# Kernel tuning notes

Hardware: AMD Instinct MI355X
Metric: run time of the kernel (lower is better)

## Reference

```python
import jax, jax.numpy as jnp
import numpy as np

B, S, M, E, H, F, V, L = 2, 2048, 1024, 512, 8, 2048, 8192, 6


def setup_inputs() -> dict:
    key = jax.random.key(0)
    ks = iter(jax.random.split(key, 32))
    n = lambda shape, s=0.02: jax.random.normal(next(ks), shape, jnp.float32) * s
    return {
        "encoded": jax.random.normal(next(ks), (B, M, E), jnp.float32),
        "seq": jax.random.randint(next(ks), (B, S), 0, V, jnp.int32),
        "input_embed": n((V, E)),           # shared input/output embedding
        "pos_embed": n((S, E)),
        "output_bias": jnp.zeros((V,), jnp.float32),
        "self_in_w": n((L, 3 * E, E)), "self_in_b": jnp.zeros((L, 3 * E), jnp.float32),
        "self_out_w": n((L, E, E)), "self_out_b": jnp.zeros((L, E), jnp.float32),
        "cross_in_w": n((L, 3 * E, E)), "cross_in_b": jnp.zeros((L, 3 * E), jnp.float32),
        "cross_out_w": n((L, E, E)), "cross_out_b": jnp.zeros((L, E), jnp.float32),
        "self_norm_g": jnp.ones((L, E), jnp.float32), "self_norm_b": jnp.zeros((L, E), jnp.float32),
        "cross_norm_g": jnp.ones((L, E), jnp.float32), "cross_norm_b": jnp.zeros((L, E), jnp.float32),
        "mlp_norm_g": jnp.ones((L, E), jnp.float32), "mlp_norm_b": jnp.zeros((L, E), jnp.float32),
        "lin1_w": n((L, F, E)), "lin1_b": jnp.zeros((L, F), jnp.float32),
        "lin2_w": n((L, E, F)), "lin2_b": jnp.zeros((L, E), jnp.float32),
        "final_norm_g": jnp.ones((E,), jnp.float32), "final_norm_b": jnp.zeros((E,), jnp.float32),
    }


def _ln(x, g, b, eps=1e-5):
    m = jnp.mean(x, axis=-1, keepdims=True)
    v = jnp.mean((x - m) ** 2, axis=-1, keepdims=True)
    return (x - m) * jax.lax.rsqrt(v + eps) * g + b


def _mha(q, k, v, in_w, in_b, out_w, out_b, mask):
    # torch nn.MultiheadAttention (batch_first) with packed in_proj [3E, E]
    Ed = q.shape[-1]
    dh = Ed // H
    qp = q @ in_w[:Ed].T + in_b[:Ed]
    kp = k @ in_w[Ed:2 * Ed].T + in_b[Ed:2 * Ed]
    vp = v @ in_w[2 * Ed:].T + in_b[2 * Ed:]
    split = lambda t: t.reshape(t.shape[0], t.shape[1], H, dh).transpose(0, 2, 1, 3)
    qh, kh, vh = split(qp), split(kp), split(vp)  # [B, H, S, dh]
    scores = jnp.einsum('bhqd,bhkd->bhqk', qh, kh) / jnp.sqrt(jnp.float32(dh))
    if mask is not None:
        scores = jnp.where(mask, scores, jnp.float32(-1e9))
    attn = jax.nn.softmax(scores, axis=-1)
    o = jnp.einsum('bhqk,bhkd->bhqd', attn, vh)
    o = o.transpose(0, 2, 1, 3).reshape(q.shape[0], q.shape[1], Ed)
    return o @ out_w.T + out_b


def reference(encoded, seq, input_embed, pos_embed, output_bias,
              self_in_w, self_in_b, self_out_w, self_out_b,
              cross_in_w, cross_in_b, cross_out_w, cross_out_b,
              self_norm_g, self_norm_b, cross_norm_g, cross_norm_b,
              mlp_norm_g, mlp_norm_b, lin1_w, lin1_b, lin2_w, lin2_b,
              final_norm_g, final_norm_b):
    # TransformerDecoder.fit: teacher-forced forward (eval-mode dropout = identity)
    seq_len = seq.shape[1]
    x = input_embed[seq] + pos_embed[:seq_len]          # [B, S, E]
    causal = jnp.tril(jnp.ones((seq_len, seq_len), bool))
    for i in range(L):
        # post-norm decoder layer (norm_first=False)
        attn = _mha(x, x, x, self_in_w[i], self_in_b[i], self_out_w[i], self_out_b[i], causal)
        y = _ln(x + attn, self_norm_g[i], self_norm_b[i])
        cattn = _mha(y, encoded, encoded, cross_in_w[i], cross_in_b[i], cross_out_w[i], cross_out_b[i], None)
        y = _ln(y + cattn, cross_norm_g[i], cross_norm_b[i])
        h = jax.nn.gelu(y @ lin1_w[i].T + lin1_b[i], approximate=False)
        x = _ln(y + h @ lin2_w[i].T + lin2_b[i], mlp_norm_g[i], mlp_norm_b[i])
    x = _ln(x, final_norm_g, final_norm_b)               # decoder-final norm
    return x @ input_embed.T + output_bias               # shared output embedding
```

## Files before the change

### kernel.cpp

```cpp
#include <hip/hip_runtime.h>
#include <math.h>

typedef unsigned short u16;
typedef __attribute__((ext_vector_type(8))) unsigned short u16x8;
typedef __attribute__((ext_vector_type(8))) __bf16 bf16x8;
typedef __attribute__((ext_vector_type(4))) float f32x4;

constexpr int Bc = 2, Sc = 2048, Mc = 1024, Ec = 512, Hc = 8, DH = 64, Fc = 2048, Vc = 8192, Lc = 6;
constexpr int Nc = Bc * Sc;
constexpr int NMc = Bc * Mc;

__device__ __forceinline__ u16 f2b(float f) {
  __bf16 h = (__bf16)f;
  return __builtin_bit_cast(u16, h);
}

__device__ __forceinline__ f32x4 mfma16(bf16x8 a, bf16x8 b, f32x4 c) {
  return __builtin_amdgcn_mfma_f32_16x16x32_bf16(a, b, c, 0, 0, 0);
}

__global__ __launch_bounds__(256) void k_cvt(const float* __restrict__ s,
                                             u16* __restrict__ d, int n4) {
  int i = blockIdx.x * 256 + threadIdx.x;
  if (i >= n4) return;
  float4 v = ((const float4*)s)[i];
  unsigned lo = (unsigned)f2b(v.x) | ((unsigned)f2b(v.y) << 16);
  unsigned hi = (unsigned)f2b(v.z) | ((unsigned)f2b(v.w) << 16);
  ((uint2*)d)[i] = make_uint2(lo, hi);
}

__global__ __launch_bounds__(256) void k_embed(const int* __restrict__ seq,
                                               const float* __restrict__ emb,
                                               const float* __restrict__ pos,
                                               float* __restrict__ x,
                                               u16* __restrict__ xb) {
  int idx = blockIdx.x * 256 + threadIdx.x;
  int row = idx >> 9, e = idx & 511;
  int s = row & (Sc - 1);
  float v = emb[(size_t)seq[row] * Ec + e] + pos[(size_t)s * Ec + e];
  x[idx] = v;
  xb[idx] = f2b(v);
}

template <int BM, int BN, int ACT>
__global__ __launch_bounds__(256) void k_gemm_bf(const u16* __restrict__ A,
                                                 const u16* __restrict__ W,
                                                 const float* __restrict__ bias,
                                                 float* __restrict__ C32,
                                                 u16* __restrict__ Cb,
                                                 int K, int Mo) {
  constexpr int WM = BM / 2, WN = BN / 2, FM = WM / 16, FN = WN / 16;
  __shared__ __attribute__((aligned(16))) u16 As[2][BM * 64];
  __shared__ __attribute__((aligned(16))) u16 Bs[2][BN * 64];
  const int tid = threadIdx.x;
  const int w = tid >> 6, l = tid & 63, l15 = l & 15, l4 = l >> 4;
  const int lr = l >> 3, lc = l & 7;
  const int wr = (w >> 1) * WM, wc = (w & 1) * WN;
  const size_t row0 = (size_t)blockIdx.y * BM, col0 = (size_t)blockIdx.x * BN;
  const u16* Ab = A + row0 * K;
  const u16* Wb = W + col0 * K;
  f32x4 acc[FM][FN] = {};

  auto stage = [&](int buf, int k0) {
#pragma unroll
    for (int i = 0; i < BM / 32; ++i) {
      int sw = lr ^ ((i * 4 + w) & 7);
      int row = i * 32 + w * 8 + lr;
      const u16* ga = Ab + (size_t)row * K + k0 + ((lc ^ sw) & 7) * 8;
      __builtin_amdgcn_global_load_lds((const __attribute__((address_space(1))) void*)ga,
          (__attribute__((address_space(3))) void*)((char*)As[buf] + (i * 32 + w * 8) * 128), 16, 0, 0);
    }
#pragma unroll
    for (int i = 0; i < BN / 32; ++i) {
      int sw = lr ^ ((i * 4 + w) & 7);
      int row = i * 32 + w * 8 + lr;
      const u16* gw = Wb + (size_t)row * K + k0 + ((lc ^ sw) & 7) * 8;
      __builtin_amdgcn_global_load_lds((const __attribute__((address_space(1))) void*)gw,
          (__attribute__((address_space(3))) void*)((char*)Bs[buf] + (i * 32 + w * 8) * 128), 16, 0, 0);
    }
  };

  const int nk = K / 64;
  stage(0, 0);
  int cur = 0;
  for (int kt = 0; kt < nk; ++kt) {
    __syncthreads();
    if (kt + 1 < nk) stage(cur ^ 1, (kt + 1) * 64);
    const u16* AsC = As[cur];
    const u16* BsC = Bs[cur];
#pragma unroll
    for (int ks = 0; ks < 2; ++ks) {
      bf16x8 af[FM], bfr[FN];
#pragma unroll
      for (int m = 0; m < FM; ++m) {
        int ra = wr + m * 16 + l15;
        int sw = (l15 & 7) ^ ((wr / 8 + 2 * m + (l15 >> 3)) & 7);
        af[m] = *(const bf16x8*)&AsC[ra * 64 + ((ks * 32 + l4 * 8) ^ (sw * 8))];
      }
#pragma unroll
      for (int n = 0; n < FN; ++n) {
        int rb = wc + n * 16 + l15;
        int sw = (l15 & 7) ^ ((wc / 8 + 2 * n + (l15 >> 3)) & 7);
        bfr[n] = *(const bf16x8*)&BsC[rb * 64 + ((ks * 32 + l4 * 8) ^ (sw * 8))];
      }
#pragma unroll
      for (int m = 0; m < FM; ++m)
#pragma unroll
        for (int n = 0; n < FN; ++n)
          acc[m][n] = mfma16(af[m], bfr[n], acc[m][n]);
    }
    cur ^= 1;
  }
#pragma unroll
  for (int n = 0; n < FN; ++n) {
    size_t col = col0 + wc + n * 16 + l15;
    float bv = bias[col];
#pragma unroll
    for (int m = 0; m < FM; ++m)
#pragma unroll
      for (int r = 0; r < 4; ++r) {
        size_t row = row0 + wr + m * 16 + l4 * 4 + r;
        float v = acc[m][n][r] + bv;
        if (ACT) v = 0.5f * v * (1.f + erff(v * 0.70710678118654752f));
        if (C32) C32[row * Mo + col] = v;
        if (Cb) Cb[row * Mo + col] = f2b(v);
      }
  }
}

__global__ __launch_bounds__(512, 4) void k_flash(const u16* __restrict__ Qp, int sq,
                                                  const u16* __restrict__ Kp,
                                                  const u16* __restrict__ Vp, int skv,
                                                  u16* __restrict__ Op, int so,
                                                  int Sq, int Sk, int causal) {
  __shared__ __attribute__((aligned(16))) u16 Kst[4][64 * 64];
  __shared__ __attribute__((aligned(16))) u16 Vt[4][64 * 64];
  __shared__ __attribute__((aligned(16))) u16 Pl[8][16 * 64];
  const int tid = threadIdx.x;
  const int w = tid >> 6, l = tid & 63, l15 = l & 15, l4 = l >> 4;
  const int wq = w & 3, ws = w >> 2;
  const int lr = l >> 3, lc = l & 7;
  const int t256 = tid & 255;
  const int kk2 = t256 >> 3, dblk = tid & 7;
  const int nqt = Sq / 64, nkt = Sk / 64;
  const int h = blockIdx.y, b = blockIdx.z;
  const int bx = blockIdx.x;
  const int qi = causal ? ((b & 1) ? bx : (nqt - 1 - bx)) : bx;
  const int qt0 = qi * 64;
  const int nt = causal ? (qi + 1) : nkt;
  const int NI = (nt + 1) >> 1;
  const u16* Qb = Qp + (size_t)b * Sq * sq + h * DH;
  const u16* Kb = Kp + (size_t)b * Sk * skv + h * DH;
  const u16* Vb = Vp + (size_t)b * Sk * skv + h * DH;

  bf16x8 qf[2];
  {
    const u16* qp0 = Qb + (size_t)(qt0 + wq * 16 + l15) * sq + l4 * 8;
    qf[0] = *(const bf16x8*)(qp0);
    qf[1] = *(const bf16x8*)(qp0 + 32);
  }
  bf16x8 onesf;
#pragma unroll
  for (int j = 0; j < 8; ++j) onesf[j] = (__bf16)1.0f;

  f32x4 oacc[4] = {};
  f32x4 lsacc = {0.f, 0.f, 0.f, 0.f};
  float Mx[4];
#pragma unroll
  for (int r = 0; r < 4; ++r) Mx[r] = -3e38f;

  const float CSC = 0.18033688011112042f;

  u16x8 va, vbv;
  auto stageK = [&](int slot, int kt) {
#pragma unroll
    for (int i = 0; i < 2; ++i) {
      int sw = lr ^ ((i * 4 + wq) & 7);
      int row = i * 32 + wq * 8 + lr;
      const u16* src = Kb + (size_t)(kt + row) * skv + ((lc ^ sw) & 7) * 8;
      __builtin_amdgcn_global_load_lds((const __attribute__((address_space(1))) void*)src,
          (__attribute__((address_space(3))) void*)((char*)Kst[slot] + (i * 32 + wq * 8) * 128), 16, 0, 0);
    }
  };
  auto loadV = [&](int kt) {
    const u16* vp0 = Vb + (size_t)(kt + 2 * kk2) * skv + dblk * 8;
    va = *(const u16x8*)vp0;
    vbv = *(const u16x8*)(vp0 + skv);
  };
  auto writeV = [&](int slot) {
    char* Vb_ = (char*)Vt[slot];
#pragma unroll
    for (int j = 0; j < 8; ++j) {
      int d = dblk * 8 + j;
      int sw = (j ^ dblk) & 7;
      unsigned pk = (unsigned)va[j] | ((unsigned)vbv[j] << 16);
      *(unsigned*)(Vb_ + d * 128 + ((4 * kk2) ^ (sw << 4))) = pk;
    }
  };

  stageK(ws * 2, ws * 64);
  loadV(ws * 64);
  writeV(ws * 2);
  asm volatile("s_waitcnt lgkmcnt(0)" ::: "memory");
  __builtin_amdgcn_sched_barrier(0);
  __builtin_amdgcn_s_barrier();

  u16* Pw = Pl[w];
  for (int i = 0; i < NI; ++i) {
    const int t = 2 * i + ws;
    const int tn = 2 * (i + 1) + ws;
    const int cur = ws * 2 + (i & 1);
    const int nxt = ws * 2 + ((i + 1) & 1);
    const bool haveNext = tn < nt;
    if (haveNext) {
      stageK(nxt, tn * 64);
      loadV(tn * 64);
    }
    const bool act = t < nt;
    if (act) {
      const u16* KstC = Kst[cur];
      const u16* VtC = Vt[cur];

      f32x4 sf[4] = {};
      __builtin_amdgcn_s_setprio(1);
#pragma unroll
      for (int n = 0; n < 4; ++n) {
        int rk = n * 16 + l15;
        int sw = (l15 & 7) ^ ((2 * n + (l15 >> 3)) & 7);
#pragma unroll
        for (int ks = 0; ks < 2; ++ks) {
          bf16x8 kf = *(const bf16x8*)&KstC[rk * 64 + ((ks * 32 + l4 * 8) ^ (sw * 8))];
          sf[n] = mfma16(qf[ks], kf, sf[n]);
        }
      }
      __builtin_amdgcn_s_setprio(0);

      if (causal && t == nt - 1) {
#pragma unroll
        for (int n = 0; n < 4; ++n)
#pragma unroll
          for (int r = 0; r < 4; ++r) {
            int qrow = qt0 + wq * 16 + l4 * 4 + r;
            int kcol = t * 64 + n * 16 + l15;
            if (kcol > qrow) sf[n][r] = -3e38f;
          }
      }

      float al[4];
#pragma unroll
      for (int r = 0; r < 4; ++r) {
        float tm = fmaxf(fmaxf(sf[0][r], sf[1][r]), fmaxf(sf[2][r], sf[3][r]));
        tm = fmaxf(tm, __shfl_xor(tm, 1, 64));
        tm = fmaxf(tm, __shfl_xor(tm, 2, 64));
        tm = fmaxf(tm, __shfl_xor(tm, 4, 64));
        tm = fmaxf(tm, __shfl_xor(tm, 8, 64));
        float Mn = fmaxf(Mx[r], tm);
        al[r] = exp2f((Mx[r] - Mn) * CSC);
        Mx[r] = Mn;
      }
      float mxc[4];
#pragma unroll
      for (int r = 0; r < 4; ++r) mxc[r] = Mx[r] * CSC;
#pragma unroll
      for (int n = 0; n < 4; ++n)
#pragma unroll
        for (int r = 0; r < 4; ++r) {
          float p = exp2f(sf[n][r] * CSC - mxc[r]);
          int q = l4 * 4 + r;
          int sw = (q & 7) ^ (q >> 3);
          *(u16*)((char*)Pw + q * 128 + ((2 * (n * 16 + l15)) ^ (sw << 4))) = f2b(p);
        }
      bool grow = (al[0] < 1.f) | (al[1] < 1.f) | (al[2] < 1.f) | (al[3] < 1.f);
      if (__any(grow)) {
#pragma unroll
        for (int r = 0; r < 4; ++r) {
          lsacc[r] *= al[r];
#pragma unroll
          for (int n2 = 0; n2 < 4; ++n2) oacc[n2][r] *= al[r];
        }
      }

      asm volatile("s_waitcnt lgkmcnt(0)" ::: "memory");
      __builtin_amdgcn_sched_barrier(0);

      int swp = (l15 & 7) ^ (l15 >> 3);
      __builtin_amdgcn_s_setprio(1);
#pragma unroll
      for (int ks = 0; ks < 2; ++ks) {
        bf16x8 pf = *(const bf16x8*)((char*)Pw + l15 * 128 + ((ks * 64 + l4 * 16) ^ (swp << 4)));
        lsacc = mfma16(pf, onesf, lsacc);
#pragma unroll
        for (int n2 = 0; n2 < 4; ++n2) {
          int rd = n2 * 16 + l15;
          int sw = (l15 & 7) ^ ((2 * n2 + (l15 >> 3)) & 7);
          bf16x8 vf = *(const bf16x8*)((char*)VtC + rd * 128 + ((ks * 64 + l4 * 16) ^ (sw << 4)));
          oacc[n2] = mfma16(pf, vf, oacc[n2]);
        }
      }
      __builtin_amdgcn_s_setprio(0);
    }

    if (haveNext) writeV(nxt);
    asm volatile("s_waitcnt lgkmcnt(0)" ::: "memory");
    __builtin_amdgcn_sched_barrier(0);
    __builtin_amdgcn_s_barrier();
  }

  __syncthreads();
  float* MG = (float*)&Kst[0][0];
  if (ws == 1) {
    float* p = MG + ((size_t)wq * 64 + l) * 24;
#pragma unroll
    for (int r = 0; r < 4; ++r) { p[r] = Mx[r]; p[4 + r] = lsacc[r]; }
#pragma unroll
    for (int n2 = 0; n2 < 4; ++n2)
#pragma unroll
      for (int r = 0; r < 4; ++r) p[8 + n2 * 4 + r] = oacc[n2][r];
  }
  __syncthreads();
  if (ws == 0) {
    const float* p = MG + ((size_t)wq * 64 + l) * 24;
    u16* Ob = Op + (size_t)b * Sq * so + h * DH;
#pragma unroll
    for (int r = 0; r < 4; ++r) {
      float Mb = p[r], lb = p[4 + r];
      float M = fmaxf(Mx[r], Mb);
      float aA = exp2f((Mx[r] - M) * CSC);
      float aB = exp2f((Mb - M) * CSC);
      float lsum = lsacc[r] * aA + lb * aB;
      int qrow = qt0 + wq * 16 + l4 * 4 + r;
#pragma unroll
      for (int n2 = 0; n2 < 4; ++n2) {
        float o = oacc[n2][r] * aA + p[8 + n2 * 4 + r] * aB;
        Ob[(size_t)qrow * so + n2 * 16 + l15] = f2b(o / lsum);
      }
    }
  }
}

__global__ __launch_bounds__(256) void k_res_ln(const float* __restrict__ xin,
                                                const float* __restrict__ rres,
                                                const float* __restrict__ g,
                                                const float* __restrict__ bet,
                                                float* __restrict__ outf,
                                                u16* __restrict__ outb,
                                                int has_res) {
  __shared__ float red[4];
  const int row = blockIdx.x, tid = threadIdx.x;
  const float* xr = xin + (size_t)row * Ec;
  float v0 = xr[tid], v1 = xr[tid + 256];
  if (has_res) {
    const float* rr = rres + (size_t)row * Ec;
    v0 += rr[tid];
    v1 += rr[tid + 256];
  }
  float s = v0 + v1;
#pragma unroll
  for (int o = 32; o; o >>= 1) s += __shfl_down(s, o, 64);
  if ((tid & 63) == 0) red[tid >> 6] = s;
  __syncthreads();
  const float mean = (red[0] + red[1] + red[2] + red[3]) * (1.f / Ec);
  float d0 = v0 - mean, d1 = v1 - mean;
  float vs = d0 * d0 + d1 * d1;
#pragma unroll
  for (int o = 32; o; o >>= 1) vs += __shfl_down(vs, o, 64);
  __syncthreads();
  if ((tid & 63) == 0) red[tid >> 6] = vs;
  __syncthreads();
  const float var = (red[0] + red[1] + red[2] + red[3]) * (1.f / Ec);
  const float inv = rsqrtf(var + 1e-5f);
  float o0 = d0 * inv * g[tid] + bet[tid];
  float o1 = d1 * inv * g[tid + 256] + bet[tid + 256];
  float* orow = outf + (size_t)row * Ec;
  orow[tid] = o0;
  orow[tid + 256] = o1;
  if (outb) {
    u16* brow = outb + (size_t)row * Ec;
    brow[tid] = f2b(o0);
    brow[tid + 256] = f2b(o1);
  }
}

extern "C" void kernel_launch(void* const* d_in, const int* in_sizes, int n_in,
                              void* d_out, int out_size, void* d_ws, size_t ws_size,
                              hipStream_t stream) {
  const float* encoded      = (const float*)d_in[0];
  const int*   seq          = (const int*)d_in[1];
  const float* input_embed  = (const float*)d_in[2];
  const float* pos_embed    = (const float*)d_in[3];
  const float* output_bias  = (const float*)d_in[4];
  const float* self_in_w    = (const float*)d_in[5];
  const float* self_in_b    = (const float*)d_in[6];
  const float* self_out_w   = (const float*)d_in[7];
  const float* self_out_b   = (const float*)d_in[8];
  const float* cross_in_w   = (const float*)d_in[9];
  const float* cross_in_b   = (const float*)d_in[10];
  const float* cross_out_w  = (const float*)d_in[11];
  const float* cross_out_b  = (const float*)d_in[12];
  const float* self_norm_g  = (const float*)d_in[13];
  const float* self_norm_b  = (const float*)d_in[14];
  const float* cross_norm_g = (const float*)d_in[15];
  const float* cross_norm_b = (const float*)d_in[16];
  const float* mlp_norm_g   = (const float*)d_in[17];
  const float* mlp_norm_b   = (const float*)d_in[18];
  const float* lin1_w       = (const float*)d_in[19];
  const float* lin1_b       = (const float*)d_in[20];
  const float* lin2_w       = (const float*)d_in[21];
  const float* lin2_b       = (const float*)d_in[22];
  const float* final_norm_g = (const float*)d_in[23];
  const float* final_norm_b = (const float*)d_in[24];

  char* oc = (char*)d_out;
  auto take = [&](size_t bytes) { char* p = oc; oc += bytes; return p; };
  u16* wsi  = (u16*)take((size_t)Lc * 3 * Ec * Ec * 2);
  u16* wso  = (u16*)take((size_t)Lc * Ec * Ec * 2);
  u16* wci  = (u16*)take((size_t)Lc * 3 * Ec * Ec * 2);
  u16* wco  = (u16*)take((size_t)Lc * Ec * Ec * 2);
  u16* wl1  = (u16*)take((size_t)Lc * Fc * Ec * 2);
  u16* wl2  = (u16*)take((size_t)Lc * Ec * Fc * 2);
  u16* encb = (u16*)take((size_t)NMc * Ec * 2);
  float* xs  = (float*)take((size_t)Nc * Ec * 4);
  float* ys  = (float*)take((size_t)Nc * Ec * 4);
  float* tmp = (float*)take((size_t)Nc * Ec * 4);
  u16* xbf  = (u16*)take((size_t)Nc * Ec * 2);
  u16* qkvb = (u16*)take((size_t)Nc * 3 * Ec * 2);
  u16* ctxb = (u16*)take((size_t)Nc * Ec * 2);
  u16* qxb  = (u16*)take((size_t)Nc * Ec * 2);
  u16* kvb  = (u16*)take((size_t)NMc * 2 * Ec * 2);
  u16* hbf  = (u16*)take((size_t)Nc * Fc * 2);
  u16* xfb  = (u16*)d_ws;
  u16* embb = (u16*)((char*)d_ws + (size_t)Nc * Ec * 2);

  const dim3 blk(256);
  auto cvt = [&](const float* s, u16* d, size_t n) {
    int n4 = (int)(n / 4);
    k_cvt<<<dim3((n4 + 255) / 256), blk, 0, stream>>>(s, d, n4);
  };
  cvt(self_in_w, wsi, (size_t)Lc * 3 * Ec * Ec);
  cvt(self_out_w, wso, (size_t)Lc * Ec * Ec);
  cvt(cross_in_w, wci, (size_t)Lc * 3 * Ec * Ec);
  cvt(cross_out_w, wco, (size_t)Lc * Ec * Ec);
  cvt(lin1_w, wl1, (size_t)Lc * Fc * Ec);
  cvt(lin2_w, wl2, (size_t)Lc * Ec * Fc);
  cvt(input_embed, embb, (size_t)Vc * Ec);
  cvt(encoded, encb, (size_t)NMc * Ec);

  k_embed<<<dim3(Nc * Ec / 256), blk, 0, stream>>>(seq, input_embed, pos_embed, xs, xbf);

  const dim3 gAttn(Sc / 64, Hc, Bc);
  const dim3 blkA(512);
  for (int l = 0; l < Lc; ++l) {
    const u16* wsi_l = wsi + (size_t)l * 3 * Ec * Ec;
    const u16* wci_l = wci + (size_t)l * 3 * Ec * Ec;
    k_gemm_bf<128, 128, 0><<<dim3(3 * Ec / 128, Nc / 128), blk, 0, stream>>>(
        xbf, wsi_l, self_in_b + (size_t)l * 3 * Ec, nullptr, qkvb, Ec, 3 * Ec);
    k_flash<<<gAttn, blkA, 0, stream>>>(qkvb, 3 * Ec, qkvb + Ec, qkvb + 2 * Ec, 3 * Ec,
                                        ctxb, Ec, Sc, Sc, 1);
    k_gemm_bf<128, 64, 0><<<dim3(Ec / 64, Nc / 128), blk, 0, stream>>>(
        ctxb, wso + (size_t)l * Ec * Ec, self_out_b + (size_t)l * Ec, tmp, nullptr, Ec, Ec);
    k_res_ln<<<dim3(Nc), blk, 0, stream>>>(xs, tmp, self_norm_g + (size_t)l * Ec,
                                           self_norm_b + (size_t)l * Ec, ys, xbf, 1);
    k_gemm_bf<128, 64, 0><<<dim3(Ec / 64, Nc / 128), blk, 0, stream>>>(
        xbf, wci_l, cross_in_b + (size_t)l * 3 * Ec, nullptr, qxb, Ec, Ec);
    k_gemm_bf<128, 64, 0><<<dim3(2 * Ec / 64, NMc / 128), blk, 0, stream>>>(
        encb, wci_l + (size_t)Ec * Ec, cross_in_b + (size_t)l * 3 * Ec + Ec,
        nullptr, kvb, Ec, 2 * Ec);
    k_flash<<<gAttn, blkA, 0, stream>>>(qxb, Ec, kvb, kvb + Ec, 2 * Ec,
                                        ctxb, Ec, Sc, Mc, 0);
    k_gemm_bf<128, 64, 0><<<dim3(Ec / 64, Nc / 128), blk, 0, stream>>>(
        ctxb, wco + (size_t)l * Ec * Ec, cross_out_b + (size_t)l * Ec, tmp, nullptr, Ec, Ec);
    k_res_ln<<<dim3(Nc), blk, 0, stream>>>(ys, tmp, cross_norm_g + (size_t)l * Ec,
                                           cross_norm_b + (size_t)l * Ec, xs, xbf, 1);
    k_gemm_bf<128, 128, 1><<<dim3(Fc / 128, Nc / 128), blk, 0, stream>>>(
        xbf, wl1 + (size_t)l * Fc * Ec, lin1_b + (size_t)l * Fc, nullptr, hbf, Ec, Fc);
    k_gemm_bf<128, 64, 0><<<dim3(Ec / 64, Nc / 128), blk, 0, stream>>>(
        hbf, wl2 + (size_t)l * Ec * Fc, lin2_b + (size_t)l * Ec, tmp, nullptr, Fc, Ec);
    k_res_ln<<<dim3(Nc), blk, 0, stream>>>(xs, tmp, mlp_norm_g + (size_t)l * Ec,
                                           mlp_norm_b + (size_t)l * Ec, xs, xbf, 1);
  }

  k_res_ln<<<dim3(Nc), blk, 0, stream>>>(xs, nullptr, final_norm_g, final_norm_b, xs, xfb, 0);
  k_gemm_bf<128, 128, 0><<<dim3(Vc / 128, Nc / 128), blk, 0, stream>>>(
      xfb, embb, output_bias, (float*)d_out, nullptr, Ec, Vc);
}
```

Baseline: 1.402 ms.

## Fuse weight conversions, transpose flash QK layout, vectorize LayerNorm, shrink GEMM tiles

Replaces the eight separate fp32-to-bf16 conversion launches with a single kernel that dispatches on global index. The flash-attention kernel swaps the MFMA operand order so each lane holds one query row, which cuts the row-max reduction to two shuffles and replaces the ones-matrix MFMA with a scalar row-sum. The cross-half merge now goes through LDS in a compact layout. LayerNorm uses float2 loads and stores, and several small GEMMs move to smaller tiles (64x64, or 128x64 for QKV) to launch more blocks, at the cost of less data reuse per block.

```diff
diff --git a/kernel.cpp b/kernel.cpp
--- a/kernel.cpp
+++ b/kernel.cpp
@@ -19,14 +19,40 @@
   return __builtin_amdgcn_mfma_f32_16x16x32_bf16(a, b, c, 0, 0, 0);
 }
 
-__global__ __launch_bounds__(256) void k_cvt(const float* __restrict__ s,
-                                             u16* __restrict__ d, int n4) {
+constexpr int C0 = 1179648;
+constexpr int C1 = C0 + 393216;
+constexpr int C2 = C1 + 1179648;
+constexpr int C3 = C2 + 393216;
+constexpr int C4 = C3 + 1572864;
+constexpr int C5 = C4 + 1572864;
+constexpr int C6 = C5 + 1048576;
+constexpr int C7 = C6 + 262144;
+
+__global__ __launch_bounds__(256) void k_cvt_all(
+    const float* __restrict__ s0, const float* __restrict__ s1,
+    const float* __restrict__ s2, const float* __restrict__ s3,
+    const float* __restrict__ s4, const float* __restrict__ s5,
+    const float* __restrict__ s6, const float* __restrict__ s7,
+    u16* __restrict__ d0, u16* __restrict__ d1, u16* __restrict__ d2,
+    u16* __restrict__ d3, u16* __restrict__ d4, u16* __restrict__ d5,
+    u16* __restrict__ d6, u16* __restrict__ d7) {
   int i = blockIdx.x * 256 + threadIdx.x;
-  if (i >= n4) return;
-  float4 v = ((const float4*)s)[i];
+  const float* s; u16* d; int off;
+  if (i < C3) {
+    if (i < C1) { if (i < C0) { s = s0; d = d0; off = i; }
+                  else        { s = s1; d = d1; off = i - C0; } }
+    else        { if (i < C2) { s = s2; d = d2; off = i - C1; }
+                  else        { s = s3; d = d3; off = i - C2; } }
+  } else {
+    if (i < C5) { if (i < C4) { s = s4; d = d4; off = i - C3; }
+                  else        { s = s5; d = d5; off = i - C4; } }
+    else        { if (i < C6) { s = s6; d = d6; off = i - C5; }
+                  else        { s = s7; d = d7; off = i - C6; } }
+  }
+  float4 v = ((const float4*)s)[off];
   unsigned lo = (unsigned)f2b(v.x) | ((unsigned)f2b(v.y) << 16);
   unsigned hi = (unsigned)f2b(v.z) | ((unsigned)f2b(v.w) << 16);
-  ((uint2*)d)[i] = make_uint2(lo, hi);
+  ((uint2*)d)[off] = make_uint2(lo, hi);
 }
 
 __global__ __launch_bounds__(256) void k_embed(const int* __restrict__ seq,
@@ -152,24 +178,19 @@
   const u16* Qb = Qp + (size_t)b * Sq * sq + h * DH;
   const u16* Kb = Kp + (size_t)b * Sk * skv + h * DH;
   const u16* Vb = Vp + (size_t)b * Sk * skv + h * DH;
+  const int qg = qt0 + wq * 16 + l15;
 
   bf16x8 qf[2];
   {
-    const u16* qp0 = Qb + (size_t)(qt0 + wq * 16 + l15) * sq + l4 * 8;
+    const u16* qp0 = Qb + (size_t)qg * sq + l4 * 8;
     qf[0] = *(const bf16x8*)(qp0);
     qf[1] = *(const bf16x8*)(qp0 + 32);
   }
-  bf16x8 onesf;
-#pragma unroll
-  for (int j = 0; j < 8; ++j) onesf[j] = (__bf16)1.0f;
 
   f32x4 oacc[4] = {};
-  f32x4 lsacc = {0.f, 0.f, 0.f, 0.f};
-  float Mx[4];
-#pragma unroll
-  for (int r = 0; r < 4; ++r) Mx[r] = -3e38f;
-
+  float ls = 0.f, Mx = -3e38f;
   const float CSC = 0.18033688011112042f;
+  const int swp = (l15 & 7) ^ (l15 >> 3);
 
   u16x8 va, vbv;
   auto stageK = [&](int slot, int kt) {
@@ -208,7 +229,7 @@
   u16* Pw = Pl[w];
   for (int i = 0; i < NI; ++i) {
     const int t = 2 * i + ws;
-    const int tn = 2 * (i + 1) + ws;
+    const int tn = t + 2;
     const int cur = ws * 2 + (i & 1);
     const int nxt = ws * 2 + ((i + 1) & 1);
     const bool haveNext = tn < nt;
@@ -216,8 +237,7 @@
       stageK(nxt, tn * 64);
       loadV(tn * 64);
     }
-    const bool act = t < nt;
-    if (act) {
+    if (t < nt) {
       const u16* KstC = Kst[cur];
       const u16* VtC = Vt[cur];
 
@@ -230,7 +250,7 @@
 #pragma unroll
         for (int ks = 0; ks < 2; ++ks) {
           bf16x8 kf = *(const bf16x8*)&KstC[rk * 64 + ((ks * 32 + l4 * 8) ^ (sw * 8))];
-          sf[n] = mfma16(qf[ks], kf, sf[n]);
+          sf[n] = mfma16(kf, qf[ks], sf[n]);
         }
       }
       __builtin_amdgcn_s_setprio(0);
@@ -240,55 +260,59 @@
         for (int n = 0; n < 4; ++n)
 #pragma unroll
           for (int r = 0; r < 4; ++r) {
-            int qrow = qt0 + wq * 16 + l4 * 4 + r;
-            int kcol = t * 64 + n * 16 + l15;
-            if (kcol > qrow) sf[n][r] = -3e38f;
+            int kcol = t * 64 + n * 16 + l4 * 4 + r;
+            if (kcol > qg) sf[n][r] = -3e38f;
           }
       }
 
-      float al[4];
-#pragma unroll
-      for (int r = 0; r < 4; ++r) {
-        float tm = fmaxf(fmaxf(sf[0][r], sf[1][r]), fmaxf(sf[2][r], sf[3][r]));
-        tm = fmaxf(tm, __shfl_xor(tm, 1, 64));
-        tm = fmaxf(tm, __shfl_xor(tm, 2, 64));
-        tm = fmaxf(tm, __shfl_xor(tm, 4, 64));
-        tm = fmaxf(tm, __shfl_xor(tm, 8, 64));
-        float Mn = fmaxf(Mx[r], tm);
-        al[r] = exp2f((Mx[r] - Mn) * CSC);
-        Mx[r] = Mn;
-      }
-      float mxc[4];
-#pragma unroll
-      for (int r = 0; r < 4; ++r) mxc[r] = Mx[r] * CSC;
-#pragma unroll
-      for (int n = 0; n < 4; ++n)
-#pragma unroll
-        for (int r = 0; r < 4; ++r) {
-          float p = exp2f(sf[n][r] * CSC - mxc[r]);
-          int q = l4 * 4 + r;
-          int sw = (q & 7) ^ (q >> 3);
-          *(u16*)((char*)Pw + q * 128 + ((2 * (n * 16 + l15)) ^ (sw << 4))) = f2b(p);
-        }
-      bool grow = (al[0] < 1.f) | (al[1] < 1.f) | (al[2] < 1.f) | (al[3] < 1.f);
-      if (__any(grow)) {
-#pragma unroll
-        for (int r = 0; r < 4; ++r) {
-          lsacc[r] *= al[r];
-#pragma unroll
-          for (int n2 = 0; n2 < 4; ++n2) oacc[n2][r] *= al[r];
+      float tm = fmaxf(fmaxf(fmaxf(sf[0][0], sf[0][1]), fmaxf(sf[0][2], sf[0][3])),
+                       fmaxf(fmaxf(sf[1][0], sf[1][1]), fmaxf(sf[1][2], sf[1][3])));
+      tm = fmaxf(tm, fmaxf(fmaxf(fmaxf(sf[2][0], sf[2][1]), fmaxf(sf[2][2], sf[2][3])),
+                           fmaxf(fmaxf(sf[3][0], sf[3][1]), fmaxf(sf[3][2], sf[3][3]))));
+      tm = fmaxf(tm, __shfl_xor(tm, 16, 64));
+      tm = fmaxf(tm, __shfl_xor(tm, 32, 64));
+      float Mn = fmaxf(Mx, tm);
+      float al = exp2f((Mx - Mn) * CSC);
+      Mx = Mn;
+      float mxc = Mx * CSC;
+
+      float rs = 0.f;
+#pragma unroll
+      for (int n = 0; n < 4; ++n) {
+        float p0 = exp2f(sf[n][0] * CSC - mxc);
+        float p1 = exp2f(sf[n][1] * CSC - mxc);
+        float p2 = exp2f(sf[n][2] * CSC - mxc);
+        float p3 = exp2f(sf[n][3] * CSC - mxc);
+        rs += (p0 + p1) + (p2 + p3);
+        unsigned w0 = (unsigned)f2b(p0) | ((unsigned)f2b(p1) << 16);
+        unsigned w1 = (unsigned)f2b(p2) | ((unsigned)f2b(p3) << 16);
+        int bb = (n * 32 + l4 * 8) ^ (swp << 4);
+        *(unsigned*)((char*)Pw + l15 * 128 + bb) = w0;
+        *(unsigned*)((char*)Pw + l15 * 128 + bb + 4) = w1;
+      }
+      rs += __shfl_xor(rs, 16, 64);
+      rs += __shfl_xor(rs, 32, 64);
+      ls = ls * al + rs;
+
+      if (__any(al < 1.f)) {
+        float a0 = __shfl(al, l4 * 4 + 0, 64);
+        float a1 = __shfl(al, l4 * 4 + 1, 64);
+        float a2 = __shfl(al, l4 * 4 + 2, 64);
+        float a3 = __shfl(al, l4 * 4 + 3, 64);
+#pragma unroll
+        for (int n2 = 0; n2 < 4; ++n2) {
+          oacc[n2][0] *= a0; oacc[n2][1] *= a1;
+          oacc[n2][2] *= a2; oacc[n2][3] *= a3;
         }
       }
 
       asm volatile("s_waitcnt lgkmcnt(0)" ::: "memory");
       __builtin_amdgcn_sched_barrier(0);
 
-      int swp = (l15 & 7) ^ (l15 >> 3);
       __builtin_amdgcn_s_setprio(1);
 #pragma unroll
       for (int ks = 0; ks < 2; ++ks) {
         bf16x8 pf = *(const bf16x8*)((char*)Pw + l15 * 128 + ((ks * 64 + l4 * 16) ^ (swp << 4)));
-        lsacc = mfma16(pf, onesf, lsacc);
 #pragma unroll
         for (int n2 = 0; n2 < 4; ++n2) {
           int rd = n2 * 16 + l15;
@@ -307,32 +331,36 @@
   }
 
   __syncthreads();
-  float* MG = (float*)&Kst[0][0];
+  float* OB = (float*)&Kst[0][0];
+  float* ML = (float*)&Vt[0][0];
+  if (l4 == 0) {
+    ML[ws * 64 + wq * 16 + l15] = Mx;
+    ML[128 + ws * 64 + wq * 16 + l15] = ls;
+  }
   if (ws == 1) {
-    float* p = MG + ((size_t)wq * 64 + l) * 24;
-#pragma unroll
-    for (int r = 0; r < 4; ++r) { p[r] = Mx[r]; p[4 + r] = lsacc[r]; }
 #pragma unroll
     for (int n2 = 0; n2 < 4; ++n2)
 #pragma unroll
-      for (int r = 0; r < 4; ++r) p[8 + n2 * 4 + r] = oacc[n2][r];
+      for (int r = 0; r < 4; ++r)
+        OB[(wq * 16 + l4 * 4 + r) * 64 + n2 * 16 + l15] = oacc[n2][r];
   }
   __syncthreads();
   if (ws == 0) {
-    const float* p = MG + ((size_t)wq * 64 + l) * 24;
     u16* Ob = Op + (size_t)b * Sq * so + h * DH;
 #pragma unroll
     for (int r = 0; r < 4; ++r) {
-      float Mb = p[r], lb = p[4 + r];
-      float M = fmaxf(Mx[r], Mb);
-      float aA = exp2f((Mx[r] - M) * CSC);
-      float aB = exp2f((Mb - M) * CSC);
-      float lsum = lsacc[r] * aA + lb * aB;
-      int qrow = qt0 + wq * 16 + l4 * 4 + r;
+      int qs = wq * 16 + l4 * 4 + r;
+      float mA = ML[qs], mB = ML[64 + qs];
+      float lA = ML[128 + qs], lB = ML[192 + qs];
+      float M = fmaxf(mA, mB);
+      float aA = exp2f((mA - M) * CSC);
+      float aB = exp2f((mB - M) * CSC);
+      float inv = 1.f / (lA * aA + lB * aB);
+      int qrow = qt0 + qs;
 #pragma unroll
       for (int n2 = 0; n2 < 4; ++n2) {
-        float o = oacc[n2][r] * aA + p[8 + n2 * 4 + r] * aB;
-        Ob[(size_t)qrow * so + n2 * 16 + l15] = f2b(o / lsum);
+        float o = (oacc[n2][r] * aA + OB[qs * 64 + n2 * 16 + l15] * aB) * inv;
+        Ob[(size_t)qrow * so + n2 * 16 + l15] = f2b(o);
       }
     }
   }
@@ -347,20 +375,19 @@
                                                 int has_res) {
   __shared__ float red[4];
   const int row = blockIdx.x, tid = threadIdx.x;
-  const float* xr = xin + (size_t)row * Ec;
-  float v0 = xr[tid], v1 = xr[tid + 256];
+  const float2* xr = (const float2*)(xin + (size_t)row * Ec);
+  float2 v = xr[tid];
   if (has_res) {
-    const float* rr = rres + (size_t)row * Ec;
-    v0 += rr[tid];
-    v1 += rr[tid + 256];
-  }
-  float s = v0 + v1;
+    float2 rv = ((const float2*)(rres + (size_t)row * Ec))[tid];
+    v.x += rv.x; v.y += rv.y;
+  }
+  float s = v.x + v.y;
 #pragma unroll
   for (int o = 32; o; o >>= 1) s += __shfl_down(s, o, 64);
   if ((tid & 63) == 0) red[tid >> 6] = s;
   __syncthreads();
   const float mean = (red[0] + red[1] + red[2] + red[3]) * (1.f / Ec);
-  float d0 = v0 - mean, d1 = v1 - mean;
+  float d0 = v.x - mean, d1 = v.y - mean;
   float vs = d0 * d0 + d1 * d1;
 #pragma unroll
   for (int o = 32; o; o >>= 1) vs += __shfl_down(vs, o, 64);
@@ -369,15 +396,14 @@
   __syncthreads();
   const float var = (red[0] + red[1] + red[2] + red[3]) * (1.f / Ec);
   const float inv = rsqrtf(var + 1e-5f);
-  float o0 = d0 * inv * g[tid] + bet[tid];
-  float o1 = d1 * inv * g[tid + 256] + bet[tid + 256];
-  float* orow = outf + (size_t)row * Ec;
-  orow[tid] = o0;
-  orow[tid + 256] = o1;
+  float2 gv = ((const float2*)g)[tid];
+  float2 bv = ((const float2*)bet)[tid];
+  float o0 = d0 * inv * gv.x + bv.x;
+  float o1 = d1 * inv * gv.y + bv.y;
+  ((float2*)(outf + (size_t)row * Ec))[tid] = make_float2(o0, o1);
   if (outb) {
-    u16* brow = outb + (size_t)row * Ec;
-    brow[tid] = f2b(o0);
-    brow[tid + 256] = f2b(o1);
+    unsigned pk = (unsigned)f2b(o0) | ((unsigned)f2b(o1) << 16);
+    ((unsigned*)(outb + (size_t)row * Ec))[tid] = pk;
   }
 }
 
@@ -432,18 +458,9 @@
   u16* embb = (u16*)((char*)d_ws + (size_t)Nc * Ec * 2);
 
   const dim3 blk(256);
-  auto cvt = [&](const float* s, u16* d, size_t n) {
-    int n4 = (int)(n / 4);
-    k_cvt<<<dim3((n4 + 255) / 256), blk, 0, stream>>>(s, d, n4);
-  };
-  cvt(self_in_w, wsi, (size_t)Lc * 3 * Ec * Ec);
-  cvt(self_out_w, wso, (size_t)Lc * Ec * Ec);
-  cvt(cross_in_w, wci, (size_t)Lc * 3 * Ec * Ec);
-  cvt(cross_out_w, wco, (size_t)Lc * Ec * Ec);
-  cvt(lin1_w, wl1, (size_t)Lc * Fc * Ec);
-  cvt(lin2_w, wl2, (size_t)Lc * Ec * Fc);
-  cvt(input_embed, embb, (size_t)Vc * Ec);
-  cvt(encoded, encb, (size_t)NMc * Ec);
+  k_cvt_all<<<dim3(29696), blk, 0, stream>>>(
+      self_in_w, self_out_w, cross_in_w, cross_out_w, lin1_w, lin2_w,
+      input_embed, encoded, wsi, wso, wci, wco, wl1, wl2, embb, encb);
 
   k_embed<<<dim3(Nc * Ec / 256), blk, 0, stream>>>(seq, input_embed, pos_embed, xs, xbf);
 
@@ -452,28 +469,28 @@
   for (int l = 0; l < Lc; ++l) {
     const u16* wsi_l = wsi + (size_t)l * 3 * Ec * Ec;
     const u16* wci_l = wci + (size_t)l * 3 * Ec * Ec;
-    k_gemm_bf<128, 128, 0><<<dim3(3 * Ec / 128, Nc / 128), blk, 0, stream>>>(
+    k_gemm_bf<128, 64, 0><<<dim3(3 * Ec / 64, Nc / 128), blk, 0, stream>>>(
         xbf, wsi_l, self_in_b + (size_t)l * 3 * Ec, nullptr, qkvb, Ec, 3 * Ec);
     k_flash<<<gAttn, blkA, 0, stream>>>(qkvb, 3 * Ec, qkvb + Ec, qkvb + 2 * Ec, 3 * Ec,
                                         ctxb, Ec, Sc, Sc, 1);
-    k_gemm_bf<128, 64, 0><<<dim3(Ec / 64, Nc / 128), blk, 0, stream>>>(
+    k_gemm_bf<64, 64, 0><<<dim3(Ec / 64, Nc / 64), blk, 0, stream>>>(
         ctxb, wso + (size_t)l * Ec * Ec, self_out_b + (size_t)l * Ec, tmp, nullptr, Ec, Ec);
     k_res_ln<<<dim3(Nc), blk, 0, stream>>>(xs, tmp, self_norm_g + (size_t)l * Ec,
                                            self_norm_b + (size_t)l * Ec, ys, xbf, 1);
-    k_gemm_bf<128, 64, 0><<<dim3(Ec / 64, Nc / 128), blk, 0, stream>>>(
+    k_gemm_bf<64, 64, 0><<<dim3(Ec / 64, Nc / 64), blk, 0, stream>>>(
         xbf, wci_l, cross_in_b + (size_t)l * 3 * Ec, nullptr, qxb, Ec, Ec);
-    k_gemm_bf<128, 64, 0><<<dim3(2 * Ec / 64, NMc / 128), blk, 0, stream>>>(
+    k_gemm_bf<64, 64, 0><<<dim3(2 * Ec / 64, NMc / 64), blk, 0, stream>>>(
         encb, wci_l + (size_t)Ec * Ec, cross_in_b + (size_t)l * 3 * Ec + Ec,
         nullptr, kvb, Ec, 2 * Ec);
     k_flash<<<gAttn, blkA, 0, stream>>>(qxb, Ec, kvb, kvb + Ec, 2 * Ec,
                                         ctxb, Ec, Sc, Mc, 0);
-    k_gemm_bf<128, 64, 0><<<dim3(Ec / 64, Nc / 128), blk, 0, stream>>>(
+    k_gemm_bf<64, 64, 0><<<dim3(Ec / 64, Nc / 64), blk, 0, stream>>>(
         ctxb, wco + (size_t)l * Ec * Ec, cross_out_b + (size_t)l * Ec, tmp, nullptr, Ec, Ec);
     k_res_ln<<<dim3(Nc), blk, 0, stream>>>(ys, tmp, cross_norm_g + (size_t)l * Ec,
                                            cross_norm_b + (size_t)l * Ec, xs, xbf, 1);
     k_gemm_bf<128, 128, 1><<<dim3(Fc / 128, Nc / 128), blk, 0, stream>>>(
         xbf, wl1 + (size_t)l * Fc * Ec, lin1_b + (size_t)l * Fc, nullptr, hbf, Ec, Fc);
-    k_gemm_bf<128, 64, 0><<<dim3(Ec / 64, Nc / 128), blk, 0, stream>>>(
+    k_gemm_bf<64, 64, 0><<<dim3(Ec / 64, Nc / 64), blk, 0, stream>>>(
         hbf, wl2 + (size_t)l * Ec * Fc, lin2_b + (size_t)l * Ec, tmp, nullptr, Fc, Ec);
     k_res_ln<<<dim3(Nc), blk, 0, stream>>>(xs, tmp, mlp_norm_g + (size_t)l * Ec,
                                            mlp_norm_b + (size_t)l * Ec, xs, xbf, 1);
```

New measurement: 1.177 ms. 16.0% less time.
